# Kernel optimization log

Hardware: AMD Instinct MI355X
Metric: run time of the kernel (lower is better)

The kernel has to match this reference:

```python
import jax, jax.numpy as jnp
import numpy as np

N_NODES = 100000
N_EDGES = 1250000
IN_CH = 128
OUT_CH = 64


def setup_inputs() -> dict:
    key = jax.random.key(0)
    k1, k2, k3, k4 = jax.random.split(key, 4)
    x = jax.random.normal(k1, (N_NODES, IN_CH), dtype=jnp.float32)
    edge_index = jax.random.randint(k2, (2, N_EDGES), 0, N_NODES, dtype=jnp.int64)
    edge_weight = jax.random.uniform(k3, (N_EDGES,), dtype=jnp.float32)
    # Xavier-uniform weight, zero bias (as in reset_parameters)
    limit = float(np.sqrt(6.0 / (IN_CH + OUT_CH)))
    W = jax.random.uniform(k4, (IN_CH, OUT_CH), dtype=jnp.float32, minval=-limit, maxval=limit)
    b = jnp.zeros((OUT_CH,), dtype=jnp.float32)
    return {"x": x, "edge_index": edge_index, "edge_weight": edge_weight, "W": W, "b": b}


def reference(x, edge_index, edge_weight, W, b):
    # Dense transform: [N, in] @ [in, out] -> [N, out]
    h = jnp.matmul(x, W)
    row, col = edge_index[0], edge_index[1]
    n = h.shape[0]
    # Weighted in-degree via scatter-add on destination (row)
    deg = jnp.zeros((n,), dtype=h.dtype).at[row].add(edge_weight)
    # deg^-0.5 with inf (deg==0) replaced by 0
    deg_inv_sqrt = jnp.where(deg == 0, jnp.zeros_like(deg), deg ** -0.5)
    norm = deg_inv_sqrt[row] * deg_inv_sqrt[col]  # [E]
    # Gather source features, normalize, scatter-add to destinations
    out = jnp.zeros_like(h).at[row].add(h[col] * norm[:, None])
    return out + b
```

## Files before the change

### kernel.cpp

```cpp
#include <hip/hip_runtime.h>

#define N_NODES 100000
#define N_EDGES 1250000
#define IN_CH 128
#define OUT_CH 64

#define NPB 128
#define ACCS2 33
#define NBINS 782
#define LSTRIDE 783
#define RECCAP 2048
#define NB1 384
#define B1T 512
#define BPT 384
#define CH1 ((N_EDGES + NB1 - 1) / NB1)
#define MAXU ((CH1 + B1T - 1) / B1T)
#define GEMM_BLOCKS ((N_NODES + 127) / 128)

#define QSCALE 8192.0f
#define QBIAS_F 8388608.0f
#define QBIAS_U 8388608u
#define INV_QSCALE 1.220703125e-4f
#define SCALE_DEG 33554432.0f
#define INV_SCALE_DEG 2.9802322387695312e-08f

typedef __attribute__((ext_vector_type(8))) short short8;
typedef __attribute__((ext_vector_type(4))) float f32x4;

__device__ inline unsigned int f2bf(float f) {
    unsigned int u = __float_as_uint(f);
    unsigned int r = ((u >> 16) & 1u) + 0x7FFFu;
    return (u + r) >> 16;
}
__device__ inline float bf_lo(unsigned int p) { return __uint_as_float(p << 16); }
__device__ inline float bf_hi(unsigned int p) { return __uint_as_float(p & 0xFFFF0000u); }

__device__ inline unsigned long long qpacks(unsigned int p, float sc) {
    unsigned int lo = (unsigned int)__float2int_rn(fmaf(bf_lo(p), sc, QBIAS_F));
    unsigned int hi = (unsigned int)__float2int_rn(fmaf(bf_hi(p), sc, QBIAS_F));
    return ((unsigned long long)hi << 32) | (unsigned long long)lo;
}

__global__ __launch_bounds__(256) void init_kernel(const float* __restrict__ W,
                                                   unsigned int* __restrict__ Wb) {
    int g = blockIdx.x * 256 + threadIdx.x;
    int c = g >> 8;
    int t4 = (g >> 6) & 3;
    int l = g & 63;
    int q = l >> 4, r15 = l & 15;
    unsigned int o[4];
#pragma unroll
    for (int jj = 0; jj < 4; ++jj) {
        float f0 = W[(c * 32 + q * 8 + 2 * jj)     * OUT_CH + t4 * 16 + r15];
        float f1 = W[(c * 32 + q * 8 + 2 * jj + 1) * OUT_CH + t4 * 16 + r15];
        o[jj] = f2bf(f0) | (f2bf(f1) << 16);
    }
    *(uint4*)(Wb + (size_t)g * 4) = make_uint4(o[0], o[1], o[2], o[3]);
}

__global__ __launch_bounds__(512) void fused_kernel(const float* __restrict__ x,
                                                    const unsigned int* __restrict__ Wb,
                                                    const int* __restrict__ ei,
                                                    const float* __restrict__ ew,
                                                    int* __restrict__ lscan2d,
                                                    int2* __restrict__ brec,
                                                    unsigned int* __restrict__ hs) {
    __shared__ int2 srec[CH1];
    __shared__ int shist[NBINS];
    __shared__ int sscan[NBINS + 2];
    __shared__ int ssum[256];
    const int tid = threadIdx.x;

    if (blockIdx.x < NB1) {
        for (int i = tid; i < NBINS; i += B1T) shist[i] = 0;
        __syncthreads();

        const int e0 = blockIdx.x * CH1;
        const int total = (e0 + CH1 < N_EDGES) ? CH1 : N_EDGES - e0;

        int rowv[MAXU], colv[MAXU];
        float wv[MAXU];
#pragma unroll
        for (int u = 0; u < MAXU; ++u) {
            int e = e0 + tid + u * B1T;
            bool ok = (tid + u * B1T) < total;
            rowv[u] = ok ? ei[e] : -1;
            colv[u] = ok ? ei[N_EDGES + e] : 0;
            wv[u]   = ok ? ew[e] : 0.0f;
            if (ok) atomicAdd(&shist[rowv[u] >> 7], 1);
        }
        __syncthreads();

        int a0 = 0, a1 = 0, a2 = 0, a3 = 0, part = 0;
        const int b0 = tid * 4;
        if (tid < 256) {
            a0 = (b0 + 0 < NBINS) ? shist[b0 + 0] : 0;
            a1 = (b0 + 1 < NBINS) ? shist[b0 + 1] : 0;
            a2 = (b0 + 2 < NBINS) ? shist[b0 + 2] : 0;
            a3 = (b0 + 3 < NBINS) ? shist[b0 + 3] : 0;
            part = a0 + a1 + a2 + a3;
            ssum[tid] = part;
        }
        __syncthreads();
#pragma unroll
        for (int d = 1; d < 256; d <<= 1) {
            int add = 0;
            if (tid >= d && tid < 256) add = ssum[tid - d];
            __syncthreads();
            if (tid < 256) ssum[tid] += add;
            __syncthreads();
        }
        if (tid < 256) {
            int base = ssum[tid] - part;
            if (b0 + 0 <= NBINS) sscan[b0 + 0] = base;
            if (b0 + 1 <= NBINS) sscan[b0 + 1] = base + a0;
            if (b0 + 2 <= NBINS) sscan[b0 + 2] = base + a0 + a1;
            if (b0 + 3 <= NBINS) sscan[b0 + 3] = base + a0 + a1 + a2;
        }
        __syncthreads();

        for (int i = tid; i < NBINS; i += B1T) shist[i] = 0;
        __syncthreads();

#pragma unroll
        for (int u = 0; u < MAXU; ++u) {
            if (rowv[u] >= 0) {
                int bb = rowv[u] >> 7;
                int rk = atomicAdd(&shist[bb], 1);
                srec[sscan[bb] + rk] = make_int2(((rowv[u] & 127) << 17) | colv[u],
                                                 __float_as_int(wv[u]));
            }
        }
        __syncthreads();

        for (int i = tid; i < total; i += B1T) brec[e0 + i] = srec[i];
        int* lrow = lscan2d + blockIdx.x * LSTRIDE;
        for (int i = tid; i <= NBINS; i += B1T) lrow[i] = sscan[i];
    } else {
        const int blk  = blockIdx.x - NB1;
        const int w    = tid >> 6;
        const int lane = tid & 63;
        const int q    = lane >> 4, r15 = lane & 15;
        const int node = blk * 128 + w * 16 + r15;
        const int nl   = (node < N_NODES) ? node : N_NODES - 1;
        const float* xrow = x + (size_t)nl * IN_CH;

        f32x4 acc[4];
#pragma unroll
        for (int t = 0; t < 4; ++t) acc[t] = (f32x4){0.f, 0.f, 0.f, 0.f};

#pragma unroll
        for (int c = 0; c < 4; ++c) {
            float4 xa = *(const float4*)(xrow + c * 32 + q * 8);
            float4 xb = *(const float4*)(xrow + c * 32 + q * 8 + 4);
            short8 bfrag;
            bfrag[0] = (short)f2bf(xa.x); bfrag[1] = (short)f2bf(xa.y);
            bfrag[2] = (short)f2bf(xa.z); bfrag[3] = (short)f2bf(xa.w);
            bfrag[4] = (short)f2bf(xb.x); bfrag[5] = (short)f2bf(xb.y);
            bfrag[6] = (short)f2bf(xb.z); bfrag[7] = (short)f2bf(xb.w);
#pragma unroll
            for (int t = 0; t < 4; ++t) {
                short8 afrag = *(const short8*)(Wb + (size_t)((c * 4 + t) * 64 + lane) * 4);
                acc[t] = __builtin_amdgcn_mfma_f32_16x16x32_bf16(afrag, bfrag, acc[t], 0, 0, 0);
            }
        }

        if (node < N_NODES) {
#pragma unroll
            for (int t = 0; t < 4; ++t) {
                unsigned int p0 = f2bf(acc[t][0]) | (f2bf(acc[t][1]) << 16);
                unsigned int p1 = f2bf(acc[t][2]) | (f2bf(acc[t][3]) << 16);
                *(uint2*)(hs + (size_t)node * 32 + t * 8 + q * 2) = make_uint2(p0, p1);
            }
        }
    }
}

__global__ __launch_bounds__(BPT) void binprep_kernel(const int* __restrict__ lscan2d,
                                                      const int2* __restrict__ brec,
                                                      int* __restrict__ brec2,
                                                      float* __restrict__ dis,
                                                      int* __restrict__ qcnt,
                                                      int* __restrict__ mtot) {
    __shared__ int sst[NB1];
    __shared__ int segoff[NB1];
    __shared__ int recs[RECCAP];
    __shared__ unsigned long long degcnt[NPB];
    const int t = threadIdx.x;
    const int b = blockIdx.x;

    if (t < NPB) degcnt[t] = 0ull;
    {
        int st  = lscan2d[t * LSTRIDE + b];
        int en  = lscan2d[t * LSTRIDE + b + 1];
        sst[t] = st;
        segoff[t] = en - st;
    }
    __syncthreads();
#pragma unroll
    for (int d = 1; d < NB1; d <<= 1) {
        int add = (t >= d) ? segoff[t - d] : 0;
        __syncthreads();
        segoff[t] += add;
        __syncthreads();
    }
    const int m = segoff[NB1 - 1];

    for (int p = t; p < m; p += BPT) {
        int lo = 0, hi = NB1 - 1;
        while (lo < hi) {
            int mid = (lo + hi) >> 1;
            if (segoff[mid] > p) hi = mid; else lo = mid + 1;
        }
        int excl = (lo == 0) ? 0 : segoff[lo - 1];
        int2 rec = brec[(size_t)lo * CH1 + sst[lo] + (p - excl)];
        if (p < RECCAP) recs[p] = rec.x;
        unsigned int qd = (unsigned int)__float2int_rn(__int_as_float(rec.y) * SCALE_DEG);
        atomicAdd(&degcnt[rec.x >> 17],
                  (1ull << 32) | (unsigned long long)qd);
    }
    __syncthreads();

    if (t < NPB) {
        int node = b * NPB + t;
        if (node < N_NODES) {
            unsigned long long dc = degcnt[t];
            float d = (float)(unsigned int)dc * INV_SCALE_DEG;
            dis[node]  = (d == 0.0f) ? 0.0f : (1.0f / sqrtf(d));
            qcnt[node] = (int)(dc >> 32);
        }
    }
    int mc = (m < RECCAP) ? m : RECCAP;
    if (t == 0) mtot[b] = mc;
    for (int p = t; p < mc; p += BPT)
        brec2[(size_t)b * RECCAP + p] = recs[p];
}

__global__ __launch_bounds__(512) void gather_kernel(const int* __restrict__ mtot,
                                                     const int* __restrict__ brec2,
                                                     const uint4* __restrict__ hs,
                                                     const float* __restrict__ dis,
                                                     const int* __restrict__ qcnt,
                                                     const float* __restrict__ b,
                                                     float* __restrict__ out) {
    __shared__ unsigned long long acc[NPB * ACCS2];
    const int tid = threadIdx.x;
    const int blk = blockIdx.x;
    for (int k = tid; k < NPB * ACCS2; k += 512) acc[k] = 0ull;
    __syncthreads();

    const int m = mtot[blk];
    const int rbase = blk * RECCAP;

    const int wid = tid >> 6, lane = tid & 63;
    const int sub = lane >> 3, l8 = lane & 7;

    for (int j0 = wid * 32; j0 < m; j0 += 256) {
        bool ok[4];
        int rec[4];
        uint4 p[4];
        float sc[4];
#pragma unroll
        for (int s = 0; s < 4; ++s) {
            int jj = j0 + 8 * s + sub;
            ok[s] = jj < m;
            rec[s] = ok[s] ? brec2[rbase + jj] : 0;
        }
#pragma unroll
        for (int s = 0; s < 4; ++s) {
            p[s] = ok[s] ? hs[(size_t)(rec[s] & 0x1FFFF) * 8 + l8]
                         : make_uint4(0, 0, 0, 0);
            sc[s] = ok[s] ? QSCALE * dis[rec[s] & 0x1FFFF] : 0.0f;
        }
#pragma unroll
        for (int s = 0; s < 4; ++s) {
            if (ok[s]) {
                int ba = (rec[s] >> 17) * ACCS2 + 4 * l8;
                atomicAdd(&acc[ba + 0], qpacks(p[s].x, sc[s]));
                atomicAdd(&acc[ba + 1], qpacks(p[s].y, sc[s]));
                atomicAdd(&acc[ba + 2], qpacks(p[s].z, sc[s]));
                atomicAdd(&acc[ba + 3], qpacks(p[s].w, sc[s]));
            }
        }
    }
    __syncthreads();

    const unsigned int* acc32 = (const unsigned int*)acc;
    float bc = b[lane];
    int half = lane & 1, slot = lane >> 1;
#pragma unroll 4
    for (int r = 0; r < 16; ++r) {
        int nl = wid * 16 + r;
        int node = blk * NPB + nl;
        if (node < N_NODES) {
            unsigned int raw = acc32[(nl * ACCS2 + slot) * 2 + half];
            int qsum = (int)(raw - (unsigned int)qcnt[node] * QBIAS_U);
            float di = dis[node] * INV_QSCALE;
            out[(size_t)node * OUT_CH + lane] = (float)qsum * di + bc;
        }
    }
}

extern "C" void kernel_launch(void* const* d_in, const int* in_sizes, int n_in,
                              void* d_out, int out_size, void* d_ws, size_t ws_size,
                              hipStream_t stream) {
    const float* x  = (const float*)d_in[0];
    const int*   ei = (const int*)d_in[1];
    const float* ew = (const float*)d_in[2];
    const float* W  = (const float*)d_in[3];
    const float* b  = (const float*)d_in[4];
    float* out = (float*)d_out;

    unsigned int* hs = (unsigned int*)d_ws;
    unsigned int* Wb = hs + (size_t)N_NODES * 32;
    int* lscan2d = (int*)(Wb + 4096);
    int* mtot    = lscan2d + (size_t)NB1 * LSTRIDE;
    float* dis   = (float*)(mtot + 800);
    int* qcnt    = (int*)(dis + N_NODES);
    int* brec2   = qcnt + N_NODES;
    int2* brec   = (int2*)(brec2 + (size_t)NBINS * RECCAP);
    (void)ws_size; (void)in_sizes; (void)n_in; (void)out_size;

    init_kernel<<<4, 256, 0, stream>>>(W, Wb);
    fused_kernel<<<NB1 + GEMM_BLOCKS, 512, 0, stream>>>(x, Wb, ei, ew,
                                                        lscan2d, brec, hs);
    binprep_kernel<<<NBINS, BPT, 0, stream>>>(lscan2d, brec, brec2, dis, qcnt, mtot);
    gather_kernel<<<NBINS, 512, 0, stream>>>(mtot, brec2, (const uint4*)hs,
                                             dis, qcnt, b, out);
}
```

Before: 159.7 us.

## Regroup kernels: fold W conversion into sort, co-schedule GEMM with bin prep

The W-to-bf16 packing moves into extra blocks of the edge bucketing kernel. The dense GEMM blocks move out of that kernel and into the per-bin degree/record prep kernel, which now runs 512 threads per block. This removes one launch and lets the GEMM overlap with bin prep instead of with bucketing. The risk is that the bin-prep blocks now carry the larger shared-memory footprint and 512-thread shape, which could reduce occupancy.

```diff
diff --git a/kernel.cpp b/kernel.cpp
--- a/kernel.cpp
+++ b/kernel.cpp
@@ -12,7 +12,6 @@
 #define RECCAP 2048
 #define NB1 384
 #define B1T 512
-#define BPT 384
 #define CH1 ((N_EDGES + NB1 - 1) / NB1)
 #define MAXU ((CH1 + B1T - 1) / B1T)
 #define GEMM_BLOCKS ((N_NODES + 127) / 128)
@@ -41,103 +40,167 @@
     return ((unsigned long long)hi << 32) | (unsigned long long)lo;
 }
 
-__global__ __launch_bounds__(256) void init_kernel(const float* __restrict__ W,
-                                                   unsigned int* __restrict__ Wb) {
-    int g = blockIdx.x * 256 + threadIdx.x;
-    int c = g >> 8;
-    int t4 = (g >> 6) & 3;
-    int l = g & 63;
-    int q = l >> 4, r15 = l & 15;
-    unsigned int o[4];
-#pragma unroll
-    for (int jj = 0; jj < 4; ++jj) {
-        float f0 = W[(c * 32 + q * 8 + 2 * jj)     * OUT_CH + t4 * 16 + r15];
-        float f1 = W[(c * 32 + q * 8 + 2 * jj + 1) * OUT_CH + t4 * 16 + r15];
-        o[jj] = f2bf(f0) | (f2bf(f1) << 16);
-    }
-    *(uint4*)(Wb + (size_t)g * 4) = make_uint4(o[0], o[1], o[2], o[3]);
-}
-
-__global__ __launch_bounds__(512) void fused_kernel(const float* __restrict__ x,
-                                                    const unsigned int* __restrict__ Wb,
-                                                    const int* __restrict__ ei,
-                                                    const float* __restrict__ ew,
-                                                    int* __restrict__ lscan2d,
-                                                    int2* __restrict__ brec,
-                                                    unsigned int* __restrict__ hs) {
+__global__ __launch_bounds__(B1T) void sort_kernel(const int* __restrict__ ei,
+                                                   const float* __restrict__ ew,
+                                                   const float* __restrict__ W,
+                                                   unsigned int* __restrict__ Wb,
+                                                   int* __restrict__ lscan2d,
+                                                   int2* __restrict__ brec) {
     __shared__ int2 srec[CH1];
     __shared__ int shist[NBINS];
     __shared__ int sscan[NBINS + 2];
     __shared__ int ssum[256];
     const int tid = threadIdx.x;
 
-    if (blockIdx.x < NB1) {
-        for (int i = tid; i < NBINS; i += B1T) shist[i] = 0;
+    if (blockIdx.x >= NB1) {
+        int g = (blockIdx.x - NB1) * B1T + tid;
+        if (g < 1024) {
+            int c = g >> 8;
+            int t4 = (g >> 6) & 3;
+            int l = g & 63;
+            int q = l >> 4, r15 = l & 15;
+            unsigned int o[4];
+#pragma unroll
+            for (int jj = 0; jj < 4; ++jj) {
+                float f0 = W[(c * 32 + q * 8 + 2 * jj)     * OUT_CH + t4 * 16 + r15];
+                float f1 = W[(c * 32 + q * 8 + 2 * jj + 1) * OUT_CH + t4 * 16 + r15];
+                o[jj] = f2bf(f0) | (f2bf(f1) << 16);
+            }
+            *(uint4*)(Wb + (size_t)g * 4) = make_uint4(o[0], o[1], o[2], o[3]);
+        }
+        return;
+    }
+
+    for (int i = tid; i < NBINS; i += B1T) shist[i] = 0;
+    __syncthreads();
+
+    const int e0 = blockIdx.x * CH1;
+    const int total = (e0 + CH1 < N_EDGES) ? CH1 : N_EDGES - e0;
+
+    int rowv[MAXU], colv[MAXU];
+    float wv[MAXU];
+#pragma unroll
+    for (int u = 0; u < MAXU; ++u) {
+        int e = e0 + tid + u * B1T;
+        bool ok = (tid + u * B1T) < total;
+        rowv[u] = ok ? ei[e] : -1;
+        colv[u] = ok ? ei[N_EDGES + e] : 0;
+        wv[u]   = ok ? ew[e] : 0.0f;
+        if (ok) atomicAdd(&shist[rowv[u] >> 7], 1);
+    }
+    __syncthreads();
+
+    int a0 = 0, a1 = 0, a2 = 0, a3 = 0, part = 0;
+    const int b0 = tid * 4;
+    if (tid < 256) {
+        a0 = (b0 + 0 < NBINS) ? shist[b0 + 0] : 0;
+        a1 = (b0 + 1 < NBINS) ? shist[b0 + 1] : 0;
+        a2 = (b0 + 2 < NBINS) ? shist[b0 + 2] : 0;
+        a3 = (b0 + 3 < NBINS) ? shist[b0 + 3] : 0;
+        part = a0 + a1 + a2 + a3;
+        ssum[tid] = part;
+    }
+    __syncthreads();
+#pragma unroll
+    for (int d = 1; d < 256; d <<= 1) {
+        int add = 0;
+        if (tid >= d && tid < 256) add = ssum[tid - d];
         __syncthreads();
-
-        const int e0 = blockIdx.x * CH1;
-        const int total = (e0 + CH1 < N_EDGES) ? CH1 : N_EDGES - e0;
-
-        int rowv[MAXU], colv[MAXU];
-        float wv[MAXU];
-#pragma unroll
-        for (int u = 0; u < MAXU; ++u) {
-            int e = e0 + tid + u * B1T;
-            bool ok = (tid + u * B1T) < total;
-            rowv[u] = ok ? ei[e] : -1;
-            colv[u] = ok ? ei[N_EDGES + e] : 0;
-            wv[u]   = ok ? ew[e] : 0.0f;
-            if (ok) atomicAdd(&shist[rowv[u] >> 7], 1);
-        }
+        if (tid < 256) ssum[tid] += add;
         __syncthreads();
-
-        int a0 = 0, a1 = 0, a2 = 0, a3 = 0, part = 0;
-        const int b0 = tid * 4;
-        if (tid < 256) {
-            a0 = (b0 + 0 < NBINS) ? shist[b0 + 0] : 0;
-            a1 = (b0 + 1 < NBINS) ? shist[b0 + 1] : 0;
-            a2 = (b0 + 2 < NBINS) ? shist[b0 + 2] : 0;
-            a3 = (b0 + 3 < NBINS) ? shist[b0 + 3] : 0;
-            part = a0 + a1 + a2 + a3;
-            ssum[tid] = part;
+    }
+    if (tid < 256) {
+        int base = ssum[tid] - part;
+        if (b0 + 0 <= NBINS) sscan[b0 + 0] = base;
+        if (b0 + 1 <= NBINS) sscan[b0 + 1] = base + a0;
+        if (b0 + 2 <= NBINS) sscan[b0 + 2] = base + a0 + a1;
+        if (b0 + 3 <= NBINS) sscan[b0 + 3] = base + a0 + a1 + a2;
+    }
+    __syncthreads();
+
+    for (int i = tid; i < NBINS; i += B1T) shist[i] = 0;
+    __syncthreads();
+
+#pragma unroll
+    for (int u = 0; u < MAXU; ++u) {
+        if (rowv[u] >= 0) {
+            int bb = rowv[u] >> 7;
+            int rk = atomicAdd(&shist[bb], 1);
+            srec[sscan[bb] + rk] = make_int2(((rowv[u] & 127) << 17) | colv[u],
+                                             __float_as_int(wv[u]));
+        }
+    }
+    __syncthreads();
+
+    for (int i = tid; i < total; i += B1T) brec[e0 + i] = srec[i];
+    int* lrow = lscan2d + blockIdx.x * LSTRIDE;
+    for (int i = tid; i <= NBINS; i += B1T) lrow[i] = sscan[i];
+}
+
+__global__ __launch_bounds__(512) void prep_gemm_kernel(const float* __restrict__ x,
+                                                        const unsigned int* __restrict__ Wb,
+                                                        const int* __restrict__ lscan2d,
+                                                        const int2* __restrict__ brec,
+                                                        int* __restrict__ brec2,
+                                                        float* __restrict__ dis,
+                                                        int* __restrict__ qcnt,
+                                                        int* __restrict__ mtot,
+                                                        unsigned int* __restrict__ hs) {
+    __shared__ int sst[NB1];
+    __shared__ int segoff[NB1];
+    __shared__ int recs[RECCAP];
+    __shared__ unsigned long long degcnt[NPB];
+    const int tid = threadIdx.x;
+
+    if (blockIdx.x < NBINS) {
+        const int b = blockIdx.x;
+        if (tid < NPB) degcnt[tid] = 0ull;
+        if (tid < NB1) {
+            int st = lscan2d[tid * LSTRIDE + b];
+            int en = lscan2d[tid * LSTRIDE + b + 1];
+            sst[tid] = st;
+            segoff[tid] = en - st;
         }
         __syncthreads();
 #pragma unroll
-        for (int d = 1; d < 256; d <<= 1) {
+        for (int d = 1; d < NB1; d <<= 1) {
             int add = 0;
-            if (tid >= d && tid < 256) add = ssum[tid - d];
+            if (tid >= d && tid < NB1) add = segoff[tid - d];
             __syncthreads();
-            if (tid < 256) ssum[tid] += add;
+            if (tid < NB1) segoff[tid] += add;
             __syncthreads();
         }
-        if (tid < 256) {
-            int base = ssum[tid] - part;
-            if (b0 + 0 <= NBINS) sscan[b0 + 0] = base;
-            if (b0 + 1 <= NBINS) sscan[b0 + 1] = base + a0;
-            if (b0 + 2 <= NBINS) sscan[b0 + 2] = base + a0 + a1;
-            if (b0 + 3 <= NBINS) sscan[b0 + 3] = base + a0 + a1 + a2;
+        const int m = segoff[NB1 - 1];
+
+        for (int p = tid; p < m; p += 512) {
+            int lo = 0, hi = NB1 - 1;
+            while (lo < hi) {
+                int mid = (lo + hi) >> 1;
+                if (segoff[mid] > p) hi = mid; else lo = mid + 1;
+            }
+            int excl = (lo == 0) ? 0 : segoff[lo - 1];
+            int2 rec = brec[(size_t)lo * CH1 + sst[lo] + (p - excl)];
+            if (p < RECCAP) recs[p] = rec.x;
+            unsigned int qd = (unsigned int)__float2int_rn(__int_as_float(rec.y) * SCALE_DEG);
+            atomicAdd(&degcnt[rec.x >> 17], (1ull << 32) | (unsigned long long)qd);
         }
         __syncthreads();
 
-        for (int i = tid; i < NBINS; i += B1T) shist[i] = 0;
-        __syncthreads();
-
-#pragma unroll
-        for (int u = 0; u < MAXU; ++u) {
-            if (rowv[u] >= 0) {
-                int bb = rowv[u] >> 7;
-                int rk = atomicAdd(&shist[bb], 1);
-                srec[sscan[bb] + rk] = make_int2(((rowv[u] & 127) << 17) | colv[u],
-                                                 __float_as_int(wv[u]));
-            }
-        }
-        __syncthreads();
-
-        for (int i = tid; i < total; i += B1T) brec[e0 + i] = srec[i];
-        int* lrow = lscan2d + blockIdx.x * LSTRIDE;
-        for (int i = tid; i <= NBINS; i += B1T) lrow[i] = sscan[i];
+        if (tid < NPB) {
+            int node = b * NPB + tid;
+            if (node < N_NODES) {
+                unsigned long long dc = degcnt[tid];
+                float d = (float)(unsigned int)dc * INV_SCALE_DEG;
+                dis[node]  = (d == 0.0f) ? 0.0f : (1.0f / sqrtf(d));
+                qcnt[node] = (int)(dc >> 32);
+            }
+        }
+        int mc = (m < RECCAP) ? m : RECCAP;
+        if (tid == 0) mtot[b] = mc;
+        for (int p = tid; p < mc; p += 512)
+            brec2[(size_t)b * RECCAP + p] = recs[p];
     } else {
-        const int blk  = blockIdx.x - NB1;
+        const int blk  = blockIdx.x - NBINS;
         const int w    = tid >> 6;
         const int lane = tid & 63;
         const int q    = lane >> 4, r15 = lane & 15;
@@ -174,66 +237,6 @@
             }
         }
     }
-}
-
-__global__ __launch_bounds__(BPT) void binprep_kernel(const int* __restrict__ lscan2d,
-                                                      const int2* __restrict__ brec,
-                                                      int* __restrict__ brec2,
-                                                      float* __restrict__ dis,
-                                                      int* __restrict__ qcnt,
-                                                      int* __restrict__ mtot) {
-    __shared__ int sst[NB1];
-    __shared__ int segoff[NB1];
-    __shared__ int recs[RECCAP];
-    __shared__ unsigned long long degcnt[NPB];
-    const int t = threadIdx.x;
-    const int b = blockIdx.x;
-
-    if (t < NPB) degcnt[t] = 0ull;
-    {
-        int st  = lscan2d[t * LSTRIDE + b];
-        int en  = lscan2d[t * LSTRIDE + b + 1];
-        sst[t] = st;
-        segoff[t] = en - st;
-    }
-    __syncthreads();
-#pragma unroll
-    for (int d = 1; d < NB1; d <<= 1) {
-        int add = (t >= d) ? segoff[t - d] : 0;
-        __syncthreads();
-        segoff[t] += add;
-        __syncthreads();
-    }
-    const int m = segoff[NB1 - 1];
-
-    for (int p = t; p < m; p += BPT) {
-        int lo = 0, hi = NB1 - 1;
-        while (lo < hi) {
-            int mid = (lo + hi) >> 1;
-            if (segoff[mid] > p) hi = mid; else lo = mid + 1;
-        }
-        int excl = (lo == 0) ? 0 : segoff[lo - 1];
-        int2 rec = brec[(size_t)lo * CH1 + sst[lo] + (p - excl)];
-        if (p < RECCAP) recs[p] = rec.x;
-        unsigned int qd = (unsigned int)__float2int_rn(__int_as_float(rec.y) * SCALE_DEG);
-        atomicAdd(&degcnt[rec.x >> 17],
-                  (1ull << 32) | (unsigned long long)qd);
-    }
-    __syncthreads();
-
-    if (t < NPB) {
-        int node = b * NPB + t;
-        if (node < N_NODES) {
-            unsigned long long dc = degcnt[t];
-            float d = (float)(unsigned int)dc * INV_SCALE_DEG;
-            dis[node]  = (d == 0.0f) ? 0.0f : (1.0f / sqrtf(d));
-            qcnt[node] = (int)(dc >> 32);
-        }
-    }
-    int mc = (m < RECCAP) ? m : RECCAP;
-    if (t == 0) mtot[b] = mc;
-    for (int p = t; p < mc; p += BPT)
-        brec2[(size_t)b * RECCAP + p] = recs[p];
 }
 
 __global__ __launch_bounds__(512) void gather_kernel(const int* __restrict__ mtot,
@@ -321,10 +324,10 @@
     int2* brec   = (int2*)(brec2 + (size_t)NBINS * RECCAP);
     (void)ws_size; (void)in_sizes; (void)n_in; (void)out_size;
 
-    init_kernel<<<4, 256, 0, stream>>>(W, Wb);
-    fused_kernel<<<NB1 + GEMM_BLOCKS, 512, 0, stream>>>(x, Wb, ei, ew,
-                                                        lscan2d, brec, hs);
-    binprep_kernel<<<NBINS, BPT, 0, stream>>>(lscan2d, brec, brec2, dis, qcnt, mtot);
+    sort_kernel<<<NB1 + 2, B1T, 0, stream>>>(ei, ew, W, Wb, lscan2d, brec);
+    prep_gemm_kernel<<<NBINS + GEMM_BLOCKS, 512, 0, stream>>>(x, Wb, lscan2d, brec,
+                                                              brec2, dis, qcnt,
+                                                              mtot, hs);
     gather_kernel<<<NBINS, 512, 0, stream>>>(mtot, brec2, (const uint4*)hs,
                                              dis, qcnt, b, out);
 }
```

Result: no change. 159.2 us (-0.3%).
